# Performance work log

Measured on AMD Instinct MI355X. Metric: run time of the kernel, lower is better.

The kernel has to match this reference:

```python
import jax, jax.numpy as jnp
import numpy as np

B, N, M, K, C = 16, 8192, 2048, 32, 128


def setup_inputs() -> dict:
    key = jax.random.key(0)
    k1, k2, k3, k4 = jax.random.split(key, 4)
    inp = jax.random.normal(k1, (B, N, C), dtype=jnp.float32)
    points = jax.random.normal(k2, (B, N, 3), dtype=jnp.float32)
    next_pts = jax.random.normal(k3, (B, M, 3), dtype=jnp.float32)
    indices = jax.random.randint(k4, (B, M, K), 0, N)  # precomputed KNN indices
    return {"input": inp, "points": points, "next_pts": next_pts, "indices": indices}


def reference(input, points, next_pts, indices):
    # input: [B,N,C], points: [B,N,3], next_pts: [B,M,3], indices: [B,M,K] int
    b = jnp.arange(input.shape[0])[:, None, None]  # [B,1,1] batch offsets
    features = input[b, indices]                   # [B,M,K,C] neighbor feature gather
    pts = points[b, indices] - next_pts[:, :, None, :]  # [B,M,K,3] relative coords
    # max-norm normalization over the K neighbors (norm computed on detached pts)
    sq = jnp.sum(jax.lax.stop_gradient(pts) ** 2, axis=3)  # [B,M,K]
    maxi = jnp.sqrt(jnp.max(sq, axis=2))                   # [B,M]
    maxi = jnp.where(maxi == 0, jnp.ones_like(maxi), maxi)
    pts = pts / maxi[:, :, None, None]
    return pts, features
```

## Files before the change

### kernel.cpp

```cpp
#include <hip/hip_runtime.h>

#define B_ 16
#define N_ 8192
#define M_ 2048
#define K_ 32
#define C_ 128

#define PTS_ELEMS ((size_t)B_ * M_ * K_ * 3)

typedef float v4f __attribute__((ext_vector_type(4)));

__global__ void pts_kernel(const float* __restrict__ points,
                           const float* __restrict__ next_pts,
                           const int* __restrict__ indices,
                           float* __restrict__ out_pts) {
    int t = blockIdx.x * blockDim.x + threadIdx.x;
    int bm = t >> 5;
    int m  = bm & (M_ - 1);
    int b  = bm >> 11;

    int idx = indices[t];
    const float* p  = points   + ((size_t)b * N_ + idx) * 3;
    const float* nq = next_pts + ((size_t)b * M_ + m) * 3;

    float x = p[0] - nq[0];
    float y = p[1] - nq[1];
    float z = p[2] - nq[2];
    float sq = x * x + y * y + z * z;

    float mx = sq;
    #pragma unroll
    for (int off = 1; off <= 16; off <<= 1) {
        float o = __shfl_xor(mx, off, 64);
        mx = fmaxf(mx, o);
    }
    float maxi = sqrtf(mx);
    if (maxi == 0.0f) maxi = 1.0f;

    float* o = out_pts + (size_t)t * 3;
    o[0] = x / maxi;
    o[1] = y / maxi;
    o[2] = z / maxi;
}

__global__ __launch_bounds__(256) void feat_kernel(const float* __restrict__ input,
                                                   const int* __restrict__ indices,
                                                   v4f* __restrict__ out_feat) {
    int bm  = blockIdx.x;
    int b   = bm >> 11;
    int tid = threadIdx.x;
    int c4  = tid & 31;
    int k0  = tid >> 5;

    const int* idxp  = indices + (size_t)bm * K_;
    const v4f* in_b  = (const v4f*)input + (size_t)b * ((size_t)N_ * (C_ / 4));
    v4f*       ob    = out_feat + (size_t)bm * (K_ * (C_ / 4));

    int i0 = idxp[k0];
    int i1 = idxp[k0 + 8];
    int i2 = idxp[k0 + 16];
    int i3 = idxp[k0 + 24];

    v4f v0 = in_b[(size_t)i0 * (C_ / 4) + c4];
    v4f v1 = in_b[(size_t)i1 * (C_ / 4) + c4];
    v4f v2 = in_b[(size_t)i2 * (C_ / 4) + c4];
    v4f v3 = in_b[(size_t)i3 * (C_ / 4) + c4];

    __builtin_nontemporal_store(v0, ob + ((k0     ) * (C_ / 4) + c4));
    __builtin_nontemporal_store(v1, ob + ((k0 +  8) * (C_ / 4) + c4));
    __builtin_nontemporal_store(v2, ob + ((k0 + 16) * (C_ / 4) + c4));
    __builtin_nontemporal_store(v3, ob + ((k0 + 24) * (C_ / 4) + c4));
}

extern "C" void kernel_launch(void* const* d_in, const int* in_sizes, int n_in,
                              void* d_out, int out_size, void* d_ws, size_t ws_size,
                              hipStream_t stream) {
    const float* input    = (const float*)d_in[0];
    const float* points   = (const float*)d_in[1];
    const float* next_pts = (const float*)d_in[2];
    const int*   indices  = (const int*)d_in[3];
    float* out = (float*)d_out;

    float* out_pts  = out;
    v4f*   out_feat = (v4f*)(out + PTS_ELEMS);

    {
        int total = B_ * M_ * K_;
        int block = 256;
        int grid = total / block;
        pts_kernel<<<grid, block, 0, stream>>>(points, next_pts, indices, out_pts);
    }
    {
        int grid = B_ * M_;
        int block = 256;
        feat_kernel<<<grid, block, 0, stream>>>(input, indices, out_feat);
    }
}
```

Baseline: 593.0 us.

## Fuse point normalization and feature gather into one kernel with XCD-aware block swizzle

Merges the relative-coordinate normalization kernel and the feature gather kernel into a single launch, where the first 32 threads of each block handle the points for that (b,m) row. Block indices are remapped so each group of 8 interleaved blocks maps to contiguous bm ranges, apparently so the blocks on one XCD share a batch's input rows in L2. Index loads are marked nontemporal. This removes one launch and a second read of the indices, but leaves most threads idle during the points phase and adds divergence within the block.

```diff
diff --git a/kernel.cpp b/kernel.cpp
--- a/kernel.cpp
+++ b/kernel.cpp
@@ -10,56 +10,55 @@
 
 typedef float v4f __attribute__((ext_vector_type(4)));
 
-__global__ void pts_kernel(const float* __restrict__ points,
-                           const float* __restrict__ next_pts,
-                           const int* __restrict__ indices,
-                           float* __restrict__ out_pts) {
-    int t = blockIdx.x * blockDim.x + threadIdx.x;
-    int bm = t >> 5;
-    int m  = bm & (M_ - 1);
+__global__ __launch_bounds__(256) void fused_kernel(const float* __restrict__ input,
+                                                    const float* __restrict__ points,
+                                                    const float* __restrict__ next_pts,
+                                                    const int* __restrict__ indices,
+                                                    float* __restrict__ out_pts,
+                                                    v4f* __restrict__ out_feat) {
+    int i  = blockIdx.x;
+    int bm = ((i & 7) << 12) | (i >> 3);
     int b  = bm >> 11;
+    int tid = threadIdx.x;
 
-    int idx = indices[t];
-    const float* p  = points   + ((size_t)b * N_ + idx) * 3;
-    const float* nq = next_pts + ((size_t)b * M_ + m) * 3;
+    const int* idxp = indices + (size_t)bm * K_;
 
-    float x = p[0] - nq[0];
-    float y = p[1] - nq[1];
-    float z = p[2] - nq[2];
-    float sq = x * x + y * y + z * z;
+    if (tid < K_) {
+        int k   = tid;
+        int idx = __builtin_nontemporal_load(idxp + k);
+        const float* p  = points   + ((size_t)b * N_ + idx) * 3;
+        const float* nq = next_pts + (size_t)bm * 3;
 
-    float mx = sq;
-    #pragma unroll
-    for (int off = 1; off <= 16; off <<= 1) {
-        float o = __shfl_xor(mx, off, 64);
-        mx = fmaxf(mx, o);
+        float x = p[0] - nq[0];
+        float y = p[1] - nq[1];
+        float z = p[2] - nq[2];
+        float sq = x * x + y * y + z * z;
+
+        float mx = sq;
+        #pragma unroll
+        for (int off = 1; off <= 16; off <<= 1) {
+            float o = __shfl_xor(mx, off, 64);
+            mx = fmaxf(mx, o);
+        }
+        float maxi = sqrtf(mx);
+        if (maxi == 0.0f) maxi = 1.0f;
+
+        float* o = out_pts + ((size_t)bm * K_ + k) * 3;
+        o[0] = x / maxi;
+        o[1] = y / maxi;
+        o[2] = z / maxi;
     }
-    float maxi = sqrtf(mx);
-    if (maxi == 0.0f) maxi = 1.0f;
 
-    float* o = out_pts + (size_t)t * 3;
-    o[0] = x / maxi;
-    o[1] = y / maxi;
-    o[2] = z / maxi;
-}
+    int c4 = tid & 31;
+    int k0 = tid >> 5;
 
-__global__ __launch_bounds__(256) void feat_kernel(const float* __restrict__ input,
-                                                   const int* __restrict__ indices,
-                                                   v4f* __restrict__ out_feat) {
-    int bm  = blockIdx.x;
-    int b   = bm >> 11;
-    int tid = threadIdx.x;
-    int c4  = tid & 31;
-    int k0  = tid >> 5;
+    const v4f* in_b = (const v4f*)input + (size_t)b * ((size_t)N_ * (C_ / 4));
+    v4f*       ob   = out_feat + (size_t)bm * (K_ * (C_ / 4));
 
-    const int* idxp  = indices + (size_t)bm * K_;
-    const v4f* in_b  = (const v4f*)input + (size_t)b * ((size_t)N_ * (C_ / 4));
-    v4f*       ob    = out_feat + (size_t)bm * (K_ * (C_ / 4));
-
-    int i0 = idxp[k0];
-    int i1 = idxp[k0 + 8];
-    int i2 = idxp[k0 + 16];
-    int i3 = idxp[k0 + 24];
+    int i0 = __builtin_nontemporal_load(idxp + k0);
+    int i1 = __builtin_nontemporal_load(idxp + k0 + 8);
+    int i2 = __builtin_nontemporal_load(idxp + k0 + 16);
+    int i3 = __builtin_nontemporal_load(idxp + k0 + 24);
 
     v4f v0 = in_b[(size_t)i0 * (C_ / 4) + c4];
     v4f v1 = in_b[(size_t)i1 * (C_ / 4) + c4];
@@ -84,15 +83,8 @@
     float* out_pts  = out;
     v4f*   out_feat = (v4f*)(out + PTS_ELEMS);
 
-    {
-        int total = B_ * M_ * K_;
-        int block = 256;
-        int grid = total / block;
-        pts_kernel<<<grid, block, 0, stream>>>(points, next_pts, indices, out_pts);
-    }
-    {
-        int grid = B_ * M_;
-        int block = 256;
-        feat_kernel<<<grid, block, 0, stream>>>(input, indices, out_feat);
-    }
+    int grid  = B_ * M_;
+    int block = 256;
+    fused_kernel<<<grid, block, 0, stream>>>(input, points, next_pts, indices,
+                                             out_pts, out_feat);
 }
```

Result: slower. 622.9 us (+5.0%).
